# Kernel tuning notes

Hardware: AMD Instinct MI355X
Metric: run time of the kernel (lower is better)

The kernel has to match this reference:

```python
import jax, jax.numpy as jnp
import numpy as np

N_NODES = 100000
N_EDGES = 1600000
IN_FEATS = 16
H_FEAT = 64
N_HEADS = 3
N_LAYERS = 8
NUM_CLASSES = 6
HID = H_FEAT * N_HEADS  # 192
NEG_SLOPE = 0.01  # torch F.leaky_relu default


def setup_inputs() -> dict:
    key = jax.random.key(0)
    ks = jax.random.split(key, 10)
    node_feat = jax.random.normal(ks[0], (N_NODES, IN_FEATS), dtype=jnp.float32)
    src = jax.random.randint(ks[1], (N_EDGES,), 0, N_NODES)
    dst = jax.random.randint(ks[2], (N_EDGES,), 0, N_NODES)
    # layer 1 params: per-head fc [H, out, in], attn [H, 2*out]
    W1 = jax.random.normal(ks[3], (N_HEADS, H_FEAT, IN_FEATS), dtype=jnp.float32) * 0.1
    a1 = jax.random.normal(ks[4], (N_HEADS, 2 * H_FEAT), dtype=jnp.float32) * 0.1
    # layers 2..8 params stacked: [L-1, H, out, hid]
    W = jax.random.normal(ks[5], (N_LAYERS - 1, N_HEADS, H_FEAT, HID), dtype=jnp.float32) * 0.1
    a = jax.random.normal(ks[6], (N_LAYERS - 1, N_HEADS, 2 * H_FEAT), dtype=jnp.float32) * 0.1
    fcW = jax.random.normal(ks[7], (NUM_CLASSES, HID), dtype=jnp.float32) * 0.1
    fcb = jnp.zeros((NUM_CLASSES,), dtype=jnp.float32)
    return {"node_feat": node_feat, "src": src, "dst": dst,
            "W1": W1, "a1": a1, "W": W, "a": a, "fcW": fcW, "fcb": fcb}


def _gat_layer(h, src, dst, Wl, al, n_nodes):
    """Multi-head GAT layer (merge='cat'). Wl:[H,O,I], al:[H,2O]."""
    O = Wl.shape[1]
    z = jnp.einsum('ni,hoi->nho', h, Wl)            # [N,H,O]
    a_src, a_dst = al[:, :O], al[:, O:]
    # attn_fc(cat(z_src, z_dst)) decomposed into per-node src/dst scores
    es = jnp.einsum('nho,ho->nh', z, a_src)          # [N,H]
    ed = jnp.einsum('nho,ho->nh', z, a_dst)          # [N,H]
    e = jax.nn.leaky_relu(es[src] + ed[dst], NEG_SLOPE)  # [E,H]
    # segment softmax over incoming edges of each dst node
    m = jax.ops.segment_max(e, dst, num_segments=n_nodes)
    m = jnp.where(jnp.isfinite(m), m, 0.0)
    ex = jnp.exp(e - m[dst])
    den = jax.ops.segment_sum(ex, dst, num_segments=n_nodes)
    alpha = ex / jnp.maximum(den[dst], 1e-9)          # [E,H]
    # scatter-sum aggregation of alpha-weighted source features
    hn = jax.ops.segment_sum(alpha[:, :, None] * z[src], dst, num_segments=n_nodes)  # [N,H,O]
    return hn.reshape(n_nodes, -1)                    # cat heads -> [N,H*O]


def reference(node_feat, src, dst, W1, a1, W, a, fcW, fcb):
    n = node_feat.shape[0]
    h = _gat_layer(node_feat, src, dst, W1, a1, n)
    h = jax.nn.elu(h)
    for l in range(W.shape[0]):
        h = _gat_layer(h, src, dst, W[l], a[l], n)
        h = jax.nn.elu(h)
    return h @ fcW.T + fcb
```

## Files before the change

### kernel.cpp

```cpp
#include <hip/hip_runtime.h>
#include <hip/hip_bf16.h>
#include <hip/hip_fp16.h>
#include <math.h>

#define NN 100000
#define NE 1600000
#define INF_ 16
#define HF 64
#define NH 3
#define HID 192
#define NC 6
#define NEG_SLOPE 0.01f

#define BSH 9
#define NBUCK 196
#define TILE 2048

typedef _Float16 half8 __attribute__((ext_vector_type(8)));
typedef float f32x4 __attribute__((ext_vector_type(4)));


__global__ __launch_bounds__(256) void k_bhist(const int* __restrict__ dst, int* __restrict__ bcnt) {
    __shared__ int c[NBUCK];
    int tid = threadIdx.x;
    for (int i = tid; i < NBUCK; i += 256) c[i] = 0;
    __syncthreads();
    int e0 = blockIdx.x * TILE;
    int end = min(e0 + TILE, NE);
    for (int i = e0 + tid; i < end; i += 256) atomicAdd(&c[dst[i] >> BSH], 1);
    __syncthreads();
    for (int i = tid; i < NBUCK; i += 256)
        if (c[i]) atomicAdd(&bcnt[i], c[i]);
}

__global__ __launch_bounds__(256) void k_bscan(const int* __restrict__ bcnt, int* __restrict__ bbase,
                                               int* __restrict__ gcur) {
    __shared__ int sc[256];
    int t = threadIdx.x;
    int v = (t < NBUCK) ? bcnt[t] : 0;
    sc[t] = v; __syncthreads();
    for (int off = 1; off < 256; off <<= 1) {
        int x = (t >= off) ? sc[t - off] : 0;
        __syncthreads();
        sc[t] += x;
        __syncthreads();
    }
    if (t < NBUCK) {
        bbase[t] = sc[t] - v;
        gcur[t] = sc[t] - v;
    }
    if (t == NBUCK - 1) bbase[NBUCK] = sc[t];
}

__global__ __launch_bounds__(256) void k_bucket(const int* __restrict__ src, const int* __restrict__ dst,
                                                int* __restrict__ gcur, int* __restrict__ staged) {
    __shared__ int cnt[NBUCK], base[NBUCK], cnt2[NBUCK];
    int tid = threadIdx.x;
    int e0 = blockIdx.x * TILE;
    int cntE = min(TILE, NE - e0);
    for (int i = tid; i < NBUCK; i += 256) { cnt[i] = 0; cnt2[i] = 0; }
    __syncthreads();
    int myDst[8], mySrc[8];
#pragma unroll
    for (int k = 0; k < 8; ++k) {
        int idx = tid + k * 256;
        if (idx < cntE) {
            myDst[k] = dst[e0 + idx];
            mySrc[k] = src[e0 + idx];
            atomicAdd(&cnt[myDst[k] >> BSH], 1);
        }
    }
    __syncthreads();
    for (int i = tid; i < NBUCK; i += 256) {
        if (cnt[i] > 0) base[i] = atomicAdd(&gcur[i], cnt[i]);
    }
    __syncthreads();
#pragma unroll
    for (int k = 0; k < 8; ++k) {
        int idx = tid + k * 256;
        if (idx < cntE) {
            int b = myDst[k] >> BSH;
            int r = atomicAdd(&cnt2[b], 1);
            staged[base[b] + r] = ((myDst[k] & 511) << 17) | mySrc[k];
        }
    }
}

__global__ __launch_bounds__(256) void k_bscatter(const int* __restrict__ bbase, const int* __restrict__ staged,
                                                  int* __restrict__ colb, int* __restrict__ row_ptr) {
    __shared__ int cnt[512];
    __shared__ int cur[512];
    __shared__ int ssum[256];
    int b = blockIdx.x;
    int tid = threadIdx.x;
    int beg = bbase[b];
    int end = bbase[b + 1];
    cnt[2 * tid] = 0; cnt[2 * tid + 1] = 0;
    __syncthreads();
    for (int i = beg + tid; i < end; i += 256) atomicAdd(&cnt[staged[i] >> 17], 1);
    __syncthreads();
    int a0 = cnt[2 * tid], a1 = cnt[2 * tid + 1];
    ssum[tid] = a0 + a1;
    __syncthreads();
    for (int off = 1; off < 256; off <<= 1) {
        int x = (tid >= off) ? ssum[tid - off] : 0;
        __syncthreads();
        ssum[tid] += x;
        __syncthreads();
    }
    int ex = (tid ? ssum[tid - 1] : 0);
    int c0 = beg + ex;
    int c1 = beg + ex + a0;
    cur[2 * tid] = c0;
    cur[2 * tid + 1] = c1;
    int n0 = b << BSH;
    if (n0 + 2 * tid < NN) row_ptr[n0 + 2 * tid] = c0;
    if (n0 + 2 * tid + 1 < NN) row_ptr[n0 + 2 * tid + 1] = c1;
    if (b == NBUCK - 1 && tid == 0) row_ptr[NN] = end;
    __syncthreads();
    for (int i = beg + tid; i < end; i += 256) {
        int v = staged[i];
        int pos = atomicAdd(&cur[v >> 17], 1);
        colb[pos] = (v & 0x1FFFF) * 384;
    }
}


__global__ __launch_bounds__(256) void k_cvtW(const float* __restrict__ W, __half* __restrict__ Wh, int n) {
    int i = blockIdx.x * 256 + threadIdx.x;
    if (i < n) Wh[i] = __float2half(W[i]);
}


__global__ __launch_bounds__(256) void k_prep(const float* __restrict__ W1, const float* __restrict__ a1,
                                              const float* __restrict__ W, const float* __restrict__ a,
                                              float* __restrict__ v0, __half* __restrict__ vh) {
    int bid = blockIdx.x, tid = threadIdx.x;
    if (bid == 0) {
        if (tid < 96) {
            int j = tid >> 4, k = tid & 15;
            int h = j % 3, sd = j / 3;
            float s = 0.f;
            for (int c = 0; c < 64; ++c)
                s += W1[h * 1024 + c * 16 + k] * a1[h * 128 + sd * 64 + c];
            v0[j * 16 + k] = s;
        }
    } else {
        int l = bid - 1;
        if (tid < HID) {
            int k = tid;
            __half* vt = vh + (size_t)l * 16 * HID;
            for (int j = 0; j < 6; ++j) {
                int h = j % 3, sd = j / 3;
                const float* wp = W + (size_t)l * 36864 + h * 12288 + k;
                const float* ap = a + (size_t)l * 384 + h * 128 + sd * 64;
                float s = 0.f;
                for (int c = 0; c < 64; ++c) s += wp[c * 192] * ap[c];
                __half hi = __float2half(s);
                __half lo = __float2half(s - __half2float(hi));
                vt[j * HID + k] = hi;
                vt[(j + 6) * HID + k] = lo;
            }
            for (int j = 12; j < 16; ++j) vt[j * HID + k] = __float2half(0.f);
        }
    }
}


__global__ __launch_bounds__(256) void k_transform1(const float* __restrict__ feat, const float* __restrict__ W1,
                                                    __half* __restrict__ zh) {
    int idx = blockIdx.x * 256 + threadIdx.x;
    if (idx >= (NN / 4) * 24) return;
    int n4 = idx / 24;
    int seg = idx - n4 * 24;
    int nbase = n4 * 4;
    const float* wr = W1 + seg * 8 * INF_;

    float acc[4][8];
#pragma unroll
    for (int j = 0; j < 4; ++j)
#pragma unroll
        for (int r = 0; r < 8; ++r) acc[j][r] = 0.f;

#pragma unroll
    for (int k4 = 0; k4 < 4; ++k4) {
        float4 f[4], w[8];
#pragma unroll
        for (int j = 0; j < 4; ++j) f[j] = *(const float4*)&feat[(nbase + j) * INF_ + k4 * 4];
#pragma unroll
        for (int r = 0; r < 8; ++r) w[r] = *(const float4*)&wr[r * INF_ + k4 * 4];
#pragma unroll
        for (int j = 0; j < 4; ++j)
#pragma unroll
            for (int r = 0; r < 8; ++r)
                acc[j][r] += f[j].x * w[r].x + f[j].y * w[r].y + f[j].z * w[r].z + f[j].w * w[r].w;
    }
#pragma unroll
    for (int j = 0; j < 4; ++j) {
        half8 o;
#pragma unroll
        for (int r = 0; r < 8; ++r) o[r] = (_Float16)acc[j][r];
        *(half8*)&zh[(size_t)(nbase + j) * HID + seg * 8] = o;
    }
}


__global__ __launch_bounds__(256) void k_esed1(const float* __restrict__ feat, const float* __restrict__ v0,
                                               float* __restrict__ es, float* __restrict__ ed) {
    __shared__ float sv[96];
    int tid = threadIdx.x;
    if (tid < 96) sv[tid] = v0[tid];
    __syncthreads();
    int n = blockIdx.x * 256 + tid;
    if (n >= NN) return;
    float f[16];
#pragma unroll
    for (int i = 0; i < 16; i += 4) {
        float4 t4 = *(const float4*)&feat[n * 16 + i];
        f[i] = t4.x; f[i + 1] = t4.y; f[i + 2] = t4.z; f[i + 3] = t4.w;
    }
#pragma unroll
    for (int j = 0; j < 6; ++j) {
        float s = 0.f;
#pragma unroll
        for (int k = 0; k < 16; ++k) s += f[k] * sv[j * 16 + k];
        if (j < 3) es[n * 3 + j] = s;
        else ed[n * 3 + (j - 3)] = s;
    }
}


__global__ __launch_bounds__(256) void k_mfma(const __half* __restrict__ Ah, const __half* __restrict__ Whl,
                                              const __half* __restrict__ vhl,
                                              __half* __restrict__ zh, float* __restrict__ es,
                                              float* __restrict__ ed) {
    __shared__ char Bs[73728];
    int tid = threadIdx.x;

#pragma unroll
    for (int i = 0; i < 18; ++i) {
        int idx = tid + i * 256;
        int row = idx / 24;
        int pos = idx - row * 24;
        uint4 v = *(const uint4*)((const char*)Whl + (size_t)idx * 16);
        *(uint4*)(Bs + row * 384 + ((pos * 16) ^ ((row & 7) << 4))) = v;
    }
    __syncthreads();

    int wid = tid >> 6;
    int lane = tid & 63;
    int lrow = lane & 15;
    int lk = lane >> 4;
    int r0 = blockIdx.x * 128 + wid * 32;

    int arow0 = min(r0 + lrow, NN - 1);
    int arow1 = min(r0 + 16 + lrow, NN - 1);
    const __half* ap0 = &Ah[(size_t)arow0 * HID];
    const __half* ap1 = &Ah[(size_t)arow1 * HID];

    f32x4 acc[2][12];
    f32x4 acc13[2];
#pragma unroll
    for (int f = 0; f < 2; ++f) {
        acc13[f] = (f32x4){0.f, 0.f, 0.f, 0.f};
#pragma unroll
        for (int t = 0; t < 12; ++t) acc[f][t] = (f32x4){0.f, 0.f, 0.f, 0.f};
    }

#pragma unroll
    for (int ks = 0; ks < 6; ++ks) {
        half8 a0 = *(const half8*)&ap0[ks * 32 + lk * 8];
        half8 a1 = *(const half8*)&ap1[ks * 32 + lk * 8];
        half8 b13 = *(const half8*)&vhl[lrow * HID + ks * 32 + lk * 8];
        acc13[0] = __builtin_amdgcn_mfma_f32_16x16x32_f16(a0, b13, acc13[0], 0, 0, 0);
        acc13[1] = __builtin_amdgcn_mfma_f32_16x16x32_f16(a1, b13, acc13[1], 0, 0, 0);
#pragma unroll
        for (int t = 0; t < 12; ++t) {
            int brow = t * 16 + lrow;
            half8 bf = *(const half8*)(Bs + brow * 384 + ((ks * 64 + lk * 16) ^ ((brow & 7) << 4)));
            acc[0][t] = __builtin_amdgcn_mfma_f32_16x16x32_f16(a0, bf, acc[0][t], 0, 0, 0);
            acc[1][t] = __builtin_amdgcn_mfma_f32_16x16x32_f16(a1, bf, acc[1][t], 0, 0, 0);
        }
    }

#pragma unroll
    for (int f = 0; f < 2; ++f) {
        int orow0 = r0 + f * 16 + lk * 4;
#pragma unroll
        for (int t = 0; t < 12; ++t) {
#pragma unroll
            for (int g = 0; g < 4; ++g) {
                int row = orow0 + g;
                if (row < NN) zh[(size_t)row * HID + t * 16 + lrow] = __float2half(acc[f][t][g]);
            }
        }
#pragma unroll
        for (int g = 0; g < 4; ++g) {
            float vhi = acc13[f][g];
            float vlo = __shfl(vhi, lane + 6);
            float tot = vhi + vlo;
            int row = orow0 + g;
            if (row < NN) {
                if (lrow < 3) es[row * NH + lrow] = tot;
                else if (lrow < 6) ed[row * NH + (lrow - 3)] = tot;
            }
        }
    }
}


__global__ __launch_bounds__(256) void k_agg(const __half* __restrict__ zh, const int* __restrict__ colb,
                                             const float* __restrict__ es, const float* __restrict__ ed,
                                             const int* __restrict__ row_ptr, __half* __restrict__ h_out) {
    int w = blockIdx.x * 4 + (threadIdx.x >> 6);
    int slot = (threadIdx.x >> 3) & 7;
    int q = threadIdx.x & 7;
    int n = w * 8 + slot;
    int beg = row_ptr[n];
    int deg = row_ptr[n + 1] - beg;

    float3 d3 = *(const float3*)((const char*)ed + n * 12);

    float l0 = 0.f, l1 = 0.f, l2 = 0.f;
    float a0[8], a1[8], a2[8];
#pragma unroll
    for (int k = 0; k < 8; ++k) { a0[k] = 0.f; a1[k] = 0.f; a2[k] = 0.f; }

    const int* cp = colb + beg;
    const char* zb = (const char*)zh + q * 16;

    int soA = 0, soB = 0;
    float3 sA = make_float3(0.f, 0.f, 0.f), sB = sA;
    if (deg > 0) { soA = cp[0]; sA = *(const float3*)((const char*)es + (soA >> 5)); }
    if (deg > 1) { soB = cp[1]; sB = *(const float3*)((const char*)es + (soB >> 5)); }

    int i = 0;
    for (; i + 2 <= deg; i += 2) {
        const char* zpA = zb + soA;
        const char* zpB = zb + soB;
        half8 zA0 = *(const half8*)(zpA);
        half8 zA1 = *(const half8*)(zpA + 128);
        half8 zA2 = *(const half8*)(zpA + 256);
        half8 zB0 = *(const half8*)(zpB);
        half8 zB1 = *(const half8*)(zpB + 128);
        half8 zB2 = *(const half8*)(zpB + 256);
        float xA0 = sA.x + d3.x, xA1 = sA.y + d3.y, xA2 = sA.z + d3.z;
        float xB0 = sB.x + d3.x, xB1 = sB.y + d3.y, xB2 = sB.z + d3.z;
        xA0 = fmaxf(xA0, NEG_SLOPE * xA0); xA1 = fmaxf(xA1, NEG_SLOPE * xA1); xA2 = fmaxf(xA2, NEG_SLOPE * xA2);
        xB0 = fmaxf(xB0, NEG_SLOPE * xB0); xB1 = fmaxf(xB1, NEG_SLOPE * xB1); xB2 = fmaxf(xB2, NEG_SLOPE * xB2);
        float pA0 = __expf(xA0), pA1 = __expf(xA1), pA2 = __expf(xA2);
        float pB0 = __expf(xB0), pB1 = __expf(xB1), pB2 = __expf(xB2);
        if (i + 2 < deg) { soA = cp[i + 2]; sA = *(const float3*)((const char*)es + (soA >> 5)); }
        if (i + 3 < deg) { soB = cp[i + 3]; sB = *(const float3*)((const char*)es + (soB >> 5)); }
        l0 += pA0 + pB0; l1 += pA1 + pB1; l2 += pA2 + pB2;
#pragma unroll
        for (int k = 0; k < 8; ++k) {
            a0[k] += pA0 * (float)zA0[k] + pB0 * (float)zB0[k];
            a1[k] += pA1 * (float)zA1[k] + pB1 * (float)zB1[k];
            a2[k] += pA2 * (float)zA2[k] + pB2 * (float)zB2[k];
        }
    }
    if (i < deg) {
        const char* zpA = zb + soA;
        half8 zA0 = *(const half8*)(zpA);
        half8 zA1 = *(const half8*)(zpA + 128);
        half8 zA2 = *(const half8*)(zpA + 256);
        float xA0 = sA.x + d3.x, xA1 = sA.y + d3.y, xA2 = sA.z + d3.z;
        xA0 = fmaxf(xA0, NEG_SLOPE * xA0); xA1 = fmaxf(xA1, NEG_SLOPE * xA1); xA2 = fmaxf(xA2, NEG_SLOPE * xA2);
        float pA0 = __expf(xA0), pA1 = __expf(xA1), pA2 = __expf(xA2);
        l0 += pA0; l1 += pA1; l2 += pA2;
#pragma unroll
        for (int k = 0; k < 8; ++k) {
            a0[k] += pA0 * (float)zA0[k];
            a1[k] += pA1 * (float)zA1[k];
            a2[k] += pA2 * (float)zA2[k];
        }
    }

    float r0 = 1.f / fmaxf(l0, 1e-9f);
    float r1 = 1.f / fmaxf(l1, 1e-9f);
    float r2 = 1.f / fmaxf(l2, 1e-9f);
    char* ob = (char*)h_out + (size_t)n * 384 + q * 16;
    union { float4 f4; __half2 h2[4]; } u;
#pragma unroll
    for (int k = 0; k < 4; ++k) {
        float x0 = a0[2 * k] * r0, x1 = a0[2 * k + 1] * r0;
        x0 = (x0 > 0.f) ? x0 : (__expf(x0) - 1.f);
        x1 = (x1 > 0.f) ? x1 : (__expf(x1) - 1.f);
        u.h2[k] = __floats2half2_rn(x0, x1);
    }
    *(float4*)ob = u.f4;
#pragma unroll
    for (int k = 0; k < 4; ++k) {
        float x0 = a1[2 * k] * r1, x1 = a1[2 * k + 1] * r1;
        x0 = (x0 > 0.f) ? x0 : (__expf(x0) - 1.f);
        x1 = (x1 > 0.f) ? x1 : (__expf(x1) - 1.f);
        u.h2[k] = __floats2half2_rn(x0, x1);
    }
    *(float4*)(ob + 128) = u.f4;
#pragma unroll
    for (int k = 0; k < 4; ++k) {
        float x0 = a2[2 * k] * r2, x1 = a2[2 * k + 1] * r2;
        x0 = (x0 > 0.f) ? x0 : (__expf(x0) - 1.f);
        x1 = (x1 > 0.f) ? x1 : (__expf(x1) - 1.f);
        u.h2[k] = __floats2half2_rn(x0, x1);
    }
    *(float4*)(ob + 256) = u.f4;
}


__device__ inline float wred_sum(float v) {
#pragma unroll
    for (int o = 32; o; o >>= 1) v += __shfl_xor(v, o);
    return v;
}

__global__ __launch_bounds__(256) void k_fc(const __half* __restrict__ hbuf, const float* __restrict__ fcW,
                                            const float* __restrict__ fcb, float* __restrict__ out) {
    __shared__ float sW[NC * HID];
    __shared__ float sb[NC];
    int tid = threadIdx.x;
    for (int i = tid; i < NC * HID; i += 256) sW[i] = fcW[i];
    if (tid < NC) sb[tid] = fcb[tid];
    __syncthreads();
    int w = tid >> 6;
    int lane = tid & 63;
    int n = blockIdx.x * 4 + w;
    if (n >= NN) return;
    float h0 = __half2float(hbuf[(size_t)n * HID + lane]);
    float h1 = __half2float(hbuf[(size_t)n * HID + 64 + lane]);
    float h2 = __half2float(hbuf[(size_t)n * HID + 128 + lane]);
#pragma unroll
    for (int j = 0; j < NC; ++j) {
        float p = h0 * sW[j * HID + lane] + h1 * sW[j * HID + 64 + lane] + h2 * sW[j * HID + 128 + lane];
        p = wred_sum(p);
        if (lane == 0) out[n * NC + j] = p + sb[j];
    }
}


extern "C" void kernel_launch(void* const* d_in, const int* in_sizes, int n_in,
                              void* d_out, int out_size, void* d_ws, size_t ws_size,
                              hipStream_t stream) {
    const float* node_feat = (const float*)d_in[0];
    const int* src = (const int*)d_in[1];
    const int* dst = (const int*)d_in[2];
    const float* W1 = (const float*)d_in[3];
    const float* a1 = (const float*)d_in[4];
    const float* W = (const float*)d_in[5];
    const float* a = (const float*)d_in[6];
    const float* fcW = (const float*)d_in[7];
    const float* fcb = (const float*)d_in[8];
    float* out = (float*)d_out;

    char* p = (char*)d_ws;
    auto alloc = [&](size_t bytes) {
        void* r = (void*)p;
        p += (bytes + 255) & ~(size_t)255;
        return r;
    };
    int* row_ptr = (int*)alloc((NN + 1) * 4);
    int* bcnt = (int*)alloc(NBUCK * 4);
    int* bbase = (int*)alloc((NBUCK + 1) * 4);
    int* gcur = (int*)alloc(NBUCK * 4);
    int* staged = (int*)alloc((size_t)NE * 4);
    int* colb = (int*)alloc((size_t)NE * 4);
    float* es = (float*)alloc((size_t)NN * NH * 4);
    float* ed = (float*)alloc((size_t)NN * NH * 4);
    __half* zh = (__half*)alloc((size_t)NN * HID * 2);
    __half* hb = (__half*)alloc((size_t)NN * HID * 2);
    const int NWH = 7 * NH * HF * HID;
    __half* Wh = (__half*)alloc((size_t)NWH * 2);
    float* v0 = (float*)alloc(96 * 4);
    __half* vh = (__half*)alloc((size_t)7 * 16 * HID * 2);

    int nb = (NN + 255) / 256;
    int gTile = (NE + TILE - 1) / TILE;

    hipMemsetAsync(bcnt, 0, NBUCK * 4, stream);
    k_bhist<<<gTile, 256, 0, stream>>>(dst, bcnt);
    k_bscan<<<1, 256, 0, stream>>>(bcnt, bbase, gcur);
    k_bucket<<<gTile, 256, 0, stream>>>(src, dst, gcur, staged);
    k_bscatter<<<NBUCK, 256, 0, stream>>>(bbase, staged, colb, row_ptr);
    k_cvtW<<<(NWH + 255) / 256, 256, 0, stream>>>(W, Wh, NWH);
    k_prep<<<8, 256, 0, stream>>>(W1, a1, W, a, v0, vh);

    int gAgg = NN / 8 / 4;
    int gT1 = ((NN / 4) * 24 + 255) / 256;

    k_transform1<<<gT1, 256, 0, stream>>>(node_feat, W1, zh);
    k_esed1<<<nb, 256, 0, stream>>>(node_feat, v0, es, ed);
    k_agg<<<gAgg, 256, 0, stream>>>(zh, colb, es, ed, row_ptr, hb);

    for (int l = 0; l < 7; ++l) {
        k_mfma<<<(NN + 127) / 128, 256, 0, stream>>>(hb, Wh + (size_t)l * NH * HF * HID,
                                                     vh + (size_t)l * 16 * HID, zh, es, ed);
        k_agg<<<gAgg, 256, 0, stream>>>(zh, colb, es, ed, row_ptr, hb);
    }

    k_fc<<<(NN + 3) / 4, 256, 0, stream>>>(hb, fcW, fcb, out);
}
```

Measured before the change: 1.206 ms.

## Sort nodes by degree and widen aggregation to 32 lanes per node

```diff
diff --git a/kernel.cpp b/kernel.cpp
--- a/kernel.cpp
+++ b/kernel.cpp
@@ -122,6 +122,46 @@
         int v = staged[i];
         int pos = atomicAdd(&cur[v >> 17], 1);
         colb[pos] = (v & 0x1FFFF) * 384;
+    }
+}
+
+
+__global__ __launch_bounds__(256) void k_dhist(const int* __restrict__ row_ptr, int* __restrict__ dh) {
+    __shared__ int c[256];
+    int tid = threadIdx.x;
+    c[tid] = 0;
+    __syncthreads();
+    int n = blockIdx.x * 256 + tid;
+    if (n < NN) {
+        int d = row_ptr[n + 1] - row_ptr[n];
+        atomicAdd(&c[min(d, 255)], 1);
+    }
+    __syncthreads();
+    if (c[tid]) atomicAdd(&dh[tid], c[tid]);
+}
+
+__global__ __launch_bounds__(256) void k_dscan(const int* __restrict__ dh, int* __restrict__ dcur) {
+    __shared__ int sc[256];
+    int t = threadIdx.x;
+    int rb = 255 - t;
+    int v = dh[rb];
+    sc[t] = v; __syncthreads();
+    for (int off = 1; off < 256; off <<= 1) {
+        int x = (t >= off) ? sc[t - off] : 0;
+        __syncthreads();
+        sc[t] += x;
+        __syncthreads();
+    }
+    dcur[rb] = sc[t] - v;
+}
+
+__global__ __launch_bounds__(256) void k_dscatter(const int* __restrict__ row_ptr, int* __restrict__ dcur,
+                                                  int* __restrict__ order) {
+    int n = blockIdx.x * 256 + threadIdx.x;
+    if (n < NN) {
+        int d = row_ptr[n + 1] - row_ptr[n];
+        int pos = atomicAdd(&dcur[min(d, 255)], 1);
+        order[pos] = n;
     }
 }
 
@@ -311,101 +351,61 @@
 
 __global__ __launch_bounds__(256) void k_agg(const __half* __restrict__ zh, const int* __restrict__ colb,
                                              const float* __restrict__ es, const float* __restrict__ ed,
-                                             const int* __restrict__ row_ptr, __half* __restrict__ h_out) {
+                                             const int* __restrict__ row_ptr, const int* __restrict__ order,
+                                             __half* __restrict__ h_out) {
     int w = blockIdx.x * 4 + (threadIdx.x >> 6);
-    int slot = (threadIdx.x >> 3) & 7;
-    int q = threadIdx.x & 7;
-    int n = w * 8 + slot;
+    int lane = threadIdx.x & 63;
+    int slot = lane >> 5;
+    int sub = lane & 31;
+    int n = order[w * 2 + slot];
     int beg = row_ptr[n];
     int deg = row_ptr[n + 1] - beg;
+    int head = sub >> 3;
+    bool act = sub < 24;
 
     float3 d3 = *(const float3*)((const char*)ed + n * 12);
-
-    float l0 = 0.f, l1 = 0.f, l2 = 0.f;
-    float a0[8], a1[8], a2[8];
-#pragma unroll
-    for (int k = 0; k < 8; ++k) { a0[k] = 0.f; a1[k] = 0.f; a2[k] = 0.f; }
+    float dv = (head == 0) ? d3.x : (head == 1) ? d3.y : d3.z;
 
     const int* cp = colb + beg;
-    const char* zb = (const char*)zh + q * 16;
-
-    int soA = 0, soB = 0;
-    float3 sA = make_float3(0.f, 0.f, 0.f), sB = sA;
-    if (deg > 0) { soA = cp[0]; sA = *(const float3*)((const char*)es + (soA >> 5)); }
-    if (deg > 1) { soB = cp[1]; sB = *(const float3*)((const char*)es + (soB >> 5)); }
-
-    int i = 0;
-    for (; i + 2 <= deg; i += 2) {
-        const char* zpA = zb + soA;
-        const char* zpB = zb + soB;
-        half8 zA0 = *(const half8*)(zpA);
-        half8 zA1 = *(const half8*)(zpA + 128);
-        half8 zA2 = *(const half8*)(zpA + 256);
-        half8 zB0 = *(const half8*)(zpB);
-        half8 zB1 = *(const half8*)(zpB + 128);
-        half8 zB2 = *(const half8*)(zpB + 256);
-        float xA0 = sA.x + d3.x, xA1 = sA.y + d3.y, xA2 = sA.z + d3.z;
-        float xB0 = sB.x + d3.x, xB1 = sB.y + d3.y, xB2 = sB.z + d3.z;
-        xA0 = fmaxf(xA0, NEG_SLOPE * xA0); xA1 = fmaxf(xA1, NEG_SLOPE * xA1); xA2 = fmaxf(xA2, NEG_SLOPE * xA2);
-        xB0 = fmaxf(xB0, NEG_SLOPE * xB0); xB1 = fmaxf(xB1, NEG_SLOPE * xB1); xB2 = fmaxf(xB2, NEG_SLOPE * xB2);
-        float pA0 = __expf(xA0), pA1 = __expf(xA1), pA2 = __expf(xA2);
-        float pB0 = __expf(xB0), pB1 = __expf(xB1), pB2 = __expf(xB2);
-        if (i + 2 < deg) { soA = cp[i + 2]; sA = *(const float3*)((const char*)es + (soA >> 5)); }
-        if (i + 3 < deg) { soB = cp[i + 3]; sB = *(const float3*)((const char*)es + (soB >> 5)); }
-        l0 += pA0 + pB0; l1 += pA1 + pB1; l2 += pA2 + pB2;
-#pragma unroll
-        for (int k = 0; k < 8; ++k) {
-            a0[k] += pA0 * (float)zA0[k] + pB0 * (float)zB0[k];
-            a1[k] += pA1 * (float)zA1[k] + pB1 * (float)zB1[k];
-            a2[k] += pA2 * (float)zA2[k] + pB2 * (float)zB2[k];
-        }
-    }
-    if (i < deg) {
-        const char* zpA = zb + soA;
-        half8 zA0 = *(const half8*)(zpA);
-        half8 zA1 = *(const half8*)(zpA + 128);
-        half8 zA2 = *(const half8*)(zpA + 256);
-        float xA0 = sA.x + d3.x, xA1 = sA.y + d3.y, xA2 = sA.z + d3.z;
-        xA0 = fmaxf(xA0, NEG_SLOPE * xA0); xA1 = fmaxf(xA1, NEG_SLOPE * xA1); xA2 = fmaxf(xA2, NEG_SLOPE * xA2);
-        float pA0 = __expf(xA0), pA1 = __expf(xA1), pA2 = __expf(xA2);
-        l0 += pA0; l1 += pA1; l2 += pA2;
-#pragma unroll
-        for (int k = 0; k < 8; ++k) {
-            a0[k] += pA0 * (float)zA0[k];
-            a1[k] += pA1 * (float)zA1[k];
-            a2[k] += pA2 * (float)zA2[k];
-        }
-    }
-
-    float r0 = 1.f / fmaxf(l0, 1e-9f);
-    float r1 = 1.f / fmaxf(l1, 1e-9f);
-    float r2 = 1.f / fmaxf(l2, 1e-9f);
-    char* ob = (char*)h_out + (size_t)n * 384 + q * 16;
-    union { float4 f4; __half2 h2[4]; } u;
-#pragma unroll
-    for (int k = 0; k < 4; ++k) {
-        float x0 = a0[2 * k] * r0, x1 = a0[2 * k + 1] * r0;
-        x0 = (x0 > 0.f) ? x0 : (__expf(x0) - 1.f);
-        x1 = (x1 > 0.f) ? x1 : (__expf(x1) - 1.f);
-        u.h2[k] = __floats2half2_rn(x0, x1);
-    }
-    *(float4*)ob = u.f4;
-#pragma unroll
-    for (int k = 0; k < 4; ++k) {
-        float x0 = a1[2 * k] * r1, x1 = a1[2 * k + 1] * r1;
-        x0 = (x0 > 0.f) ? x0 : (__expf(x0) - 1.f);
-        x1 = (x1 > 0.f) ? x1 : (__expf(x1) - 1.f);
-        u.h2[k] = __floats2half2_rn(x0, x1);
-    }
-    *(float4*)(ob + 128) = u.f4;
-#pragma unroll
-    for (int k = 0; k < 4; ++k) {
-        float x0 = a2[2 * k] * r2, x1 = a2[2 * k + 1] * r2;
-        x0 = (x0 > 0.f) ? x0 : (__expf(x0) - 1.f);
-        x1 = (x1 > 0.f) ? x1 : (__expf(x1) - 1.f);
-        u.h2[k] = __floats2half2_rn(x0, x1);
-    }
-    *(float4*)(ob + 256) = u.f4;
+    const char* zb = (const char*)zh + sub * 16;
+
+    float l = 0.f;
+    float acc[8];
+#pragma unroll
+    for (int k = 0; k < 8; ++k) acc[k] = 0.f;
+
+    int so_n = 0;
+    float3 s3_n = make_float3(0.f, 0.f, 0.f);
+    if (deg > 0) { so_n = cp[0]; s3_n = *(const float3*)((const char*)es + (so_n >> 5)); }
+
+    for (int i = 0; i < deg; ++i) {
+        int so = so_n;
+        float3 s3 = s3_n;
+        if (i + 1 < deg) { so_n = cp[i + 1]; s3_n = *(const float3*)((const char*)es + (so_n >> 5)); }
+        float sv = (head == 0) ? s3.x : (head == 1) ? s3.y : s3.z;
+        float x = sv + dv;
+        x = fmaxf(x, NEG_SLOPE * x);
+        float p = __expf(x);
+        l += p;
+        if (act) {
+            half8 z = *(const half8*)(zb + so);
+#pragma unroll
+            for (int k = 0; k < 8; ++k) acc[k] += p * (float)z[k];
+        }
+    }
+
+    if (act) {
+        float rl = 1.f / fmaxf(l, 1e-9f);
+        union { float4 f4; __half2 h2[4]; } u;
+#pragma unroll
+        for (int k = 0; k < 4; ++k) {
+            float x0 = acc[2 * k] * rl, x1 = acc[2 * k + 1] * rl;
+            x0 = (x0 > 0.f) ? x0 : (__expf(x0) - 1.f);
+            x1 = (x1 > 0.f) ? x1 : (__expf(x1) - 1.f);
+            u.h2[k] = __floats2half2_rn(x0, x1);
+        }
+        *(float4*)((char*)h_out + (size_t)n * 384 + sub * 16) = u.f4;
+    }
 }
 
 
@@ -463,6 +463,9 @@
     int* bcnt = (int*)alloc(NBUCK * 4);
     int* bbase = (int*)alloc((NBUCK + 1) * 4);
     int* gcur = (int*)alloc(NBUCK * 4);
+    int* dh = (int*)alloc(256 * 4);
+    int* dcur = (int*)alloc(256 * 4);
+    int* order = (int*)alloc((size_t)NN * 4);
     int* staged = (int*)alloc((size_t)NE * 4);
     int* colb = (int*)alloc((size_t)NE * 4);
     float* es = (float*)alloc((size_t)NN * NH * 4);
@@ -478,24 +481,28 @@
     int gTile = (NE + TILE - 1) / TILE;
 
     hipMemsetAsync(bcnt, 0, NBUCK * 4, stream);
+    hipMemsetAsync(dh, 0, 256 * 4, stream);
     k_bhist<<<gTile, 256, 0, stream>>>(dst, bcnt);
     k_bscan<<<1, 256, 0, stream>>>(bcnt, bbase, gcur);
     k_bucket<<<gTile, 256, 0, stream>>>(src, dst, gcur, staged);
     k_bscatter<<<NBUCK, 256, 0, stream>>>(bbase, staged, colb, row_ptr);
+    k_dhist<<<nb, 256, 0, stream>>>(row_ptr, dh);
+    k_dscan<<<1, 256, 0, stream>>>(dh, dcur);
+    k_dscatter<<<nb, 256, 0, stream>>>(row_ptr, dcur, order);
     k_cvtW<<<(NWH + 255) / 256, 256, 0, stream>>>(W, Wh, NWH);
     k_prep<<<8, 256, 0, stream>>>(W1, a1, W, a, v0, vh);
 
-    int gAgg = NN / 8 / 4;
+    int gAgg = NN / 2 / 4;
     int gT1 = ((NN / 4) * 24 + 255) / 256;
 
     k_transform1<<<gT1, 256, 0, stream>>>(node_feat, W1, zh);
     k_esed1<<<nb, 256, 0, stream>>>(node_feat, v0, es, ed);
-    k_agg<<<gAgg, 256, 0, stream>>>(zh, colb, es, ed, row_ptr, hb);
+    k_agg<<<gAgg, 256, 0, stream>>>(zh, colb, es, ed, row_ptr, order, hb);
 
     for (int l = 0; l < 7; ++l) {
         k_mfma<<<(NN + 127) / 128, 256, 0, stream>>>(hb, Wh + (size_t)l * NH * HF * HID,
                                                      vh + (size_t)l * 16 * HID, zh, es, ed);
-        k_agg<<<gAgg, 256, 0, stream>>>(zh, colb, es, ed, row_ptr, hb);
+        k_agg<<<gAgg, 256, 0, stream>>>(zh, colb, es, ed, row_ptr, order, hb);
     }
 
     k_fc<<<(NN + 3) / 4, 256, 0, stream>>>(hb, fcW, fcb, out);
```

After: 1.530 ms. +26.9%, slower.

## Sort nodes by in-degree within buckets to balance aggregation warps

Applied to the files above, without the earlier changes.

```diff
diff --git a/kernel.cpp b/kernel.cpp
--- a/kernel.cpp
+++ b/kernel.cpp
@@ -87,20 +87,28 @@
 }
 
 __global__ __launch_bounds__(256) void k_bscatter(const int* __restrict__ bbase, const int* __restrict__ staged,
-                                                  int* __restrict__ colb, int* __restrict__ row_ptr) {
+                                                  int* __restrict__ colb, int* __restrict__ row_ptr,
+                                                  int* __restrict__ order) {
     __shared__ int cnt[512];
     __shared__ int cur[512];
     __shared__ int ssum[256];
+    __shared__ int dh2[256];
     int b = blockIdx.x;
     int tid = threadIdx.x;
     int beg = bbase[b];
     int end = bbase[b + 1];
     cnt[2 * tid] = 0; cnt[2 * tid + 1] = 0;
+    dh2[tid] = 0;
     __syncthreads();
     for (int i = beg + tid; i < end; i += 256) atomicAdd(&cnt[staged[i] >> 17], 1);
     __syncthreads();
     int a0 = cnt[2 * tid], a1 = cnt[2 * tid + 1];
+    int n0 = b << BSH;
+    bool ok0 = (n0 + 2 * tid) < NN;
+    bool ok1 = (n0 + 2 * tid + 1) < NN;
     ssum[tid] = a0 + a1;
+    if (ok0) atomicAdd(&dh2[min(a0, 255)], 1);
+    if (ok1) atomicAdd(&dh2[min(a1, 255)], 1);
     __syncthreads();
     for (int off = 1; off < 256; off <<= 1) {
         int x = (tid >= off) ? ssum[tid - off] : 0;
@@ -113,10 +121,24 @@
     int c1 = beg + ex + a0;
     cur[2 * tid] = c0;
     cur[2 * tid + 1] = c1;
-    int n0 = b << BSH;
-    if (n0 + 2 * tid < NN) row_ptr[n0 + 2 * tid] = c0;
-    if (n0 + 2 * tid + 1 < NN) row_ptr[n0 + 2 * tid + 1] = c1;
+    if (ok0) row_ptr[n0 + 2 * tid] = c0;
+    if (ok1) row_ptr[n0 + 2 * tid + 1] = c1;
     if (b == NBUCK - 1 && tid == 0) row_ptr[NN] = end;
+    __syncthreads();
+    int rb = 255 - tid;
+    int dv = dh2[rb];
+    ssum[tid] = dv;
+    __syncthreads();
+    for (int off = 1; off < 256; off <<= 1) {
+        int x = (tid >= off) ? ssum[tid - off] : 0;
+        __syncthreads();
+        ssum[tid] += x;
+        __syncthreads();
+    }
+    dh2[rb] = ssum[tid] - dv;
+    __syncthreads();
+    if (ok0) { int r = atomicAdd(&dh2[min(a0, 255)], 1); order[n0 + r] = n0 + 2 * tid; }
+    if (ok1) { int r = atomicAdd(&dh2[min(a1, 255)], 1); order[n0 + r] = n0 + 2 * tid + 1; }
     __syncthreads();
     for (int i = beg + tid; i < end; i += 256) {
         int v = staged[i];
@@ -311,11 +333,12 @@
 
 __global__ __launch_bounds__(256) void k_agg(const __half* __restrict__ zh, const int* __restrict__ colb,
                                              const float* __restrict__ es, const float* __restrict__ ed,
-                                             const int* __restrict__ row_ptr, __half* __restrict__ h_out) {
+                                             const int* __restrict__ row_ptr, const int* __restrict__ order,
+                                             __half* __restrict__ h_out) {
     int w = blockIdx.x * 4 + (threadIdx.x >> 6);
     int slot = (threadIdx.x >> 3) & 7;
     int q = threadIdx.x & 7;
-    int n = w * 8 + slot;
+    int n = order[w * 8 + slot];
     int beg = row_ptr[n];
     int deg = row_ptr[n + 1] - beg;
 
@@ -463,6 +486,7 @@
     int* bcnt = (int*)alloc(NBUCK * 4);
     int* bbase = (int*)alloc((NBUCK + 1) * 4);
     int* gcur = (int*)alloc(NBUCK * 4);
+    int* order = (int*)alloc((size_t)NN * 4);
     int* staged = (int*)alloc((size_t)NE * 4);
     int* colb = (int*)alloc((size_t)NE * 4);
     float* es = (float*)alloc((size_t)NN * NH * 4);
@@ -481,7 +505,7 @@
     k_bhist<<<gTile, 256, 0, stream>>>(dst, bcnt);
     k_bscan<<<1, 256, 0, stream>>>(bcnt, bbase, gcur);
     k_bucket<<<gTile, 256, 0, stream>>>(src, dst, gcur, staged);
-    k_bscatter<<<NBUCK, 256, 0, stream>>>(bbase, staged, colb, row_ptr);
+    k_bscatter<<<NBUCK, 256, 0, stream>>>(bbase, staged, colb, row_ptr, order);
     k_cvtW<<<(NWH + 255) / 256, 256, 0, stream>>>(W, Wh, NWH);
     k_prep<<<8, 256, 0, stream>>>(W1, a1, W, a, v0, vh);
 
@@ -490,12 +514,12 @@
 
     k_transform1<<<gT1, 256, 0, stream>>>(node_feat, W1, zh);
     k_esed1<<<nb, 256, 0, stream>>>(node_feat, v0, es, ed);
-    k_agg<<<gAgg, 256, 0, stream>>>(zh, colb, es, ed, row_ptr, hb);
+    k_agg<<<gAgg, 256, 0, stream>>>(zh, colb, es, ed, row_ptr, order, hb);
 
     for (int l = 0; l < 7; ++l) {
         k_mfma<<<(NN + 127) / 128, 256, 0, stream>>>(hb, Wh + (size_t)l * NH * HF * HID,
                                                      vh + (size_t)l * 16 * HID, zh, es, ed);
-        k_agg<<<gAgg, 256, 0, stream>>>(zh, colb, es, ed, row_ptr, hb);
+        k_agg<<<gAgg, 256, 0, stream>>>(zh, colb, es, ed, row_ptr, order, hb);
     }
 
     k_fc<<<(NN + 3) / 4, 256, 0, stream>>>(hb, fcW, fcb, out);
```

Measured after the change: 1.390 ms. 1.15x slower.

## Prefetch A operands before barrier and stage z output through LDS for coalesced stores

Applied to the files above, without the earlier changes.

```diff
diff --git a/kernel.cpp b/kernel.cpp
--- a/kernel.cpp
+++ b/kernel.cpp
@@ -245,7 +245,6 @@
         uint4 v = *(const uint4*)((const char*)Whl + (size_t)idx * 16);
         *(uint4*)(Bs + row * 384 + ((pos * 16) ^ ((row & 7) << 4))) = v;
     }
-    __syncthreads();
 
     int wid = tid >> 6;
     int lane = tid & 63;
@@ -258,6 +257,14 @@
     const __half* ap0 = &Ah[(size_t)arow0 * HID];
     const __half* ap1 = &Ah[(size_t)arow1 * HID];
 
+    half8 a0r[6], a1r[6], b13r[6];
+#pragma unroll
+    for (int ks = 0; ks < 6; ++ks) {
+        a0r[ks] = *(const half8*)&ap0[ks * 32 + lk * 8];
+        a1r[ks] = *(const half8*)&ap1[ks * 32 + lk * 8];
+        b13r[ks] = *(const half8*)&vhl[lrow * HID + ks * 32 + lk * 8];
+    }
+
     f32x4 acc[2][12];
     f32x4 acc13[2];
 #pragma unroll
@@ -267,33 +274,24 @@
         for (int t = 0; t < 12; ++t) acc[f][t] = (f32x4){0.f, 0.f, 0.f, 0.f};
     }
 
+    __syncthreads();
+
 #pragma unroll
     for (int ks = 0; ks < 6; ++ks) {
-        half8 a0 = *(const half8*)&ap0[ks * 32 + lk * 8];
-        half8 a1 = *(const half8*)&ap1[ks * 32 + lk * 8];
-        half8 b13 = *(const half8*)&vhl[lrow * HID + ks * 32 + lk * 8];
-        acc13[0] = __builtin_amdgcn_mfma_f32_16x16x32_f16(a0, b13, acc13[0], 0, 0, 0);
-        acc13[1] = __builtin_amdgcn_mfma_f32_16x16x32_f16(a1, b13, acc13[1], 0, 0, 0);
+        acc13[0] = __builtin_amdgcn_mfma_f32_16x16x32_f16(a0r[ks], b13r[ks], acc13[0], 0, 0, 0);
+        acc13[1] = __builtin_amdgcn_mfma_f32_16x16x32_f16(a1r[ks], b13r[ks], acc13[1], 0, 0, 0);
 #pragma unroll
         for (int t = 0; t < 12; ++t) {
             int brow = t * 16 + lrow;
             half8 bf = *(const half8*)(Bs + brow * 384 + ((ks * 64 + lk * 16) ^ ((brow & 7) << 4)));
-            acc[0][t] = __builtin_amdgcn_mfma_f32_16x16x32_f16(a0, bf, acc[0][t], 0, 0, 0);
-            acc[1][t] = __builtin_amdgcn_mfma_f32_16x16x32_f16(a1, bf, acc[1][t], 0, 0, 0);
+            acc[0][t] = __builtin_amdgcn_mfma_f32_16x16x32_f16(a0r[ks], bf, acc[0][t], 0, 0, 0);
+            acc[1][t] = __builtin_amdgcn_mfma_f32_16x16x32_f16(a1r[ks], bf, acc[1][t], 0, 0, 0);
         }
     }
 
 #pragma unroll
     for (int f = 0; f < 2; ++f) {
         int orow0 = r0 + f * 16 + lk * 4;
-#pragma unroll
-        for (int t = 0; t < 12; ++t) {
-#pragma unroll
-            for (int g = 0; g < 4; ++g) {
-                int row = orow0 + g;
-                if (row < NN) zh[(size_t)row * HID + t * 16 + lrow] = __float2half(acc[f][t][g]);
-            }
-        }
 #pragma unroll
         for (int g = 0; g < 4; ++g) {
             float vhi = acc13[f][g];
@@ -305,6 +303,30 @@
                 else if (lrow < 6) ed[row * NH + (lrow - 3)] = tot;
             }
         }
+    }
+
+    __syncthreads();
+#pragma unroll
+    for (int f = 0; f < 2; ++f) {
+#pragma unroll
+        for (int t = 0; t < 12; ++t) {
+#pragma unroll
+            for (int g = 0; g < 4; ++g) {
+                int lr = wid * 32 + f * 16 + lk * 4 + g;
+                *(__half*)(Bs + lr * 384 + (t * 16 + lrow) * 2) = __float2half(acc[f][t][g]);
+            }
+        }
+    }
+    __syncthreads();
+    int rbase = blockIdx.x * 128;
+#pragma unroll
+    for (int i = 0; i < 12; ++i) {
+        int idx = tid + i * 256;
+        int row = idx / 24;
+        int pos = idx - row * 24;
+        int grow = rbase + row;
+        if (grow < NN)
+            *(uint4*)((char*)zh + (size_t)grow * 384 + pos * 16) = *(const uint4*)(Bs + idx * 16);
     }
 }
 
```

After: 1.193 ms. No clear change (-1.0%).
